# Kernel tuning notes

Measured on AMD Instinct MI355X. Metric: run time of the kernel, lower is better.

Reference implementation:

```python
import jax, jax.numpy as jnp
import numpy as np

N_NODES = 10000
IN_FEAT = 512
OUT_FEAT = 512
N_EDGES = 160000


def setup_inputs() -> dict:
    key = jax.random.key(0)
    kx, kw, ks, kd = jax.random.split(key, 4)
    x = jax.random.normal(kx, (N_NODES, IN_FEAT), dtype=jnp.float32)
    # Xavier-uniform init for w: shape [out_features, 2*in_features]
    fan_in, fan_out = 2 * IN_FEAT, OUT_FEAT
    limit = float(np.sqrt(6.0 / (fan_in + fan_out)))
    w = jax.random.uniform(kw, (OUT_FEAT, 2 * IN_FEAT), dtype=jnp.float32,
                           minval=-limit, maxval=limit)
    src = jax.random.randint(ks, (N_EDGES,), 0, N_NODES, dtype=jnp.int32)
    dst = jax.random.randint(kd, (N_EDGES,), 0, N_NODES, dtype=jnp.int32)
    edge_index = jnp.stack([src, dst], axis=0)  # [2, E]
    return {"x": x, "w": w, "edge_index": edge_index}


def reference(x, w, edge_index):
    # GraphSAGE-mean layer: h = relu(W @ concat(x, mean_{j in N(i)} x_j))
    src, dst = edge_index[0], edge_index[1]
    msgs = x[src]  # [E, F] gather of neighbor features
    summed = jax.ops.segment_sum(msgs, dst, num_segments=x.shape[0])  # [N, F]
    deg = jax.ops.segment_sum(jnp.ones_like(dst, dtype=x.dtype), dst,
                              num_segments=x.shape[0])  # [N]
    neighbor_mean = summed / jnp.maximum(deg, 1.0)[:, None]
    message = jnp.concatenate([x, neighbor_mean], axis=-1)  # [N, 2F]
    weighted = jnp.einsum('of,nf->no', w, message)  # [N, out]
    return jax.nn.relu(weighted)
```

## Files before the change

kernel.cpp:

```cpp
#include <hip/hip_runtime.h>
#include <hip/hip_bf16.h>

#define N_NODES 10000
#define IN_FEAT 512
#define OUT_FEAT 512
#define N_EDGES 160000
#define KDIM 1024
#define CAP 96

typedef __bf16 bf16x8 __attribute__((ext_vector_type(8)));
typedef float f32x4 __attribute__((ext_vector_type(4)));

#define AS1 __attribute__((address_space(1)))
#define AS3 __attribute__((address_space(3)))

__device__ __forceinline__ void async_copy16(void* lds, const void* g) {
    __builtin_amdgcn_global_load_lds((const AS1 unsigned int*)g,
                                     (AS3 unsigned int*)lds, 16, 0, 0);
}

__device__ __forceinline__ unsigned short f2bf(float f) {
    unsigned int u = __builtin_bit_cast(unsigned int, f);
    u += 0x7fffu + ((u >> 16) & 1u);
    return (unsigned short)(u >> 16);
}


__global__ __launch_bounds__(256) void k_zero(int* __restrict__ cnt) {
    int i = blockIdx.x * 256 + threadIdx.x;
    if (i < N_NODES / 4) ((int4*)cnt)[i] = (int4){0, 0, 0, 0};
}


#define PREP_EDGE_BLOCKS ((N_EDGES + 255) / 256)
#define PREP_W_BLOCKS (OUT_FEAT * KDIM / 8 / 256)
#define PREP_X_BLOCKS (N_NODES * IN_FEAT / 8 / 256)
#define PREP_BLOCKS (PREP_EDGE_BLOCKS + PREP_W_BLOCKS + PREP_X_BLOCKS)

__device__ __forceinline__ void cvt8(const float* __restrict__ src,
                                     unsigned short* __restrict__ dst, int i) {
    const float4* sp = (const float4*)(src + (size_t)i * 8);
    float4 a = sp[0], b = sp[1];
    uint4 o;
    o.x = (unsigned)f2bf(a.x) | ((unsigned)f2bf(a.y) << 16);
    o.y = (unsigned)f2bf(a.z) | ((unsigned)f2bf(a.w) << 16);
    o.z = (unsigned)f2bf(b.x) | ((unsigned)f2bf(b.y) << 16);
    o.w = (unsigned)f2bf(b.z) | ((unsigned)f2bf(b.w) << 16);
    *(uint4*)(dst + (size_t)i * 8) = o;
}

__global__ __launch_bounds__(256) void k_prep(
    const float* __restrict__ x, const float* __restrict__ w,
    const int* __restrict__ ei, int* __restrict__ cnt,
    int* __restrict__ bucket, unsigned short* __restrict__ xb,
    unsigned short* __restrict__ wb) {
    int b = blockIdx.x;
    if (b < PREP_EDGE_BLOCKS) {
        int e = b * 256 + threadIdx.x;
        if (e < N_EDGES) {
            int s = ei[e];
            int d = ei[N_EDGES + e];
            int slot = atomicAdd(&cnt[d], 1);
            if (slot < CAP) bucket[d * CAP + slot] = s;
        }
    } else if (b < PREP_EDGE_BLOCKS + PREP_W_BLOCKS) {
        int i = (b - PREP_EDGE_BLOCKS) * 256 + threadIdx.x;
        cvt8(w, wb, i);
    } else {
        int i = (b - PREP_EDGE_BLOCKS - PREP_W_BLOCKS) * 256 + threadIdx.x;
        cvt8(x, xb, i);
    }
}


__device__ __forceinline__ void accum8(float* acc, uint4 v) {
    unsigned d[4] = {v.x, v.y, v.z, v.w};
#pragma unroll
    for (int j = 0; j < 4; ++j) {
        acc[2 * j]     += __builtin_bit_cast(float, d[j] << 16);
        acc[2 * j + 1] += __builtin_bit_cast(float, d[j] & 0xffff0000u);
    }
}

__global__ __launch_bounds__(256) void k_aggregate(
    const unsigned short* __restrict__ xb, const int* __restrict__ cnt,
    const int* __restrict__ bucket, unsigned short* __restrict__ mb) {
    int wid = (blockIdx.x * 256 + threadIdx.x) >> 6;
    int lane = threadIdx.x & 63;
    if (wid >= N_NODES) return;
    int deg = cnt[wid];
    int n = deg < CAP ? deg : CAP;
    const int4* brow = (const int4*)(bucket + wid * CAP);
    const unsigned short* xrow = xb + lane * 8;
    float acc[8] = {0.f, 0.f, 0.f, 0.f, 0.f, 0.f, 0.f, 0.f};
    int e = 0;
    for (; e + 8 <= n; e += 8) {
        int4 i0 = brow[e >> 2];
        int4 i1 = brow[(e >> 2) + 1];
        uint4 v0 = *(const uint4*)(xrow + (size_t)i0.x * IN_FEAT);
        uint4 v1 = *(const uint4*)(xrow + (size_t)i0.y * IN_FEAT);
        uint4 v2 = *(const uint4*)(xrow + (size_t)i0.z * IN_FEAT);
        uint4 v3 = *(const uint4*)(xrow + (size_t)i0.w * IN_FEAT);
        uint4 v4 = *(const uint4*)(xrow + (size_t)i1.x * IN_FEAT);
        uint4 v5 = *(const uint4*)(xrow + (size_t)i1.y * IN_FEAT);
        uint4 v6 = *(const uint4*)(xrow + (size_t)i1.z * IN_FEAT);
        uint4 v7 = *(const uint4*)(xrow + (size_t)i1.w * IN_FEAT);
        accum8(acc, v0); accum8(acc, v1); accum8(acc, v2); accum8(acc, v3);
        accum8(acc, v4); accum8(acc, v5); accum8(acc, v6); accum8(acc, v7);
    }
    if (e + 4 <= n) {
        int4 i0 = brow[e >> 2];
        uint4 v0 = *(const uint4*)(xrow + (size_t)i0.x * IN_FEAT);
        uint4 v1 = *(const uint4*)(xrow + (size_t)i0.y * IN_FEAT);
        uint4 v2 = *(const uint4*)(xrow + (size_t)i0.z * IN_FEAT);
        uint4 v3 = *(const uint4*)(xrow + (size_t)i0.w * IN_FEAT);
        accum8(acc, v0); accum8(acc, v1); accum8(acc, v2); accum8(acc, v3);
        e += 4;
    }
    for (; e < n; ++e) {
        int s = bucket[wid * CAP + e];
        uint4 v = *(const uint4*)(xrow + (size_t)s * IN_FEAT);
        accum8(acc, v);
    }
    float inv = 1.0f / fmaxf((float)deg, 1.0f);
    uint4 o;
    o.x = (unsigned)f2bf(acc[0] * inv) | ((unsigned)f2bf(acc[1] * inv) << 16);
    o.y = (unsigned)f2bf(acc[2] * inv) | ((unsigned)f2bf(acc[3] * inv) << 16);
    o.z = (unsigned)f2bf(acc[4] * inv) | ((unsigned)f2bf(acc[5] * inv) << 16);
    o.w = (unsigned)f2bf(acc[6] * inv) | ((unsigned)f2bf(acc[7] * inv) << 16);
    *(uint4*)(mb + (size_t)wid * IN_FEAT + lane * 8) = o;
}


#define BM 64
#define BN 128
#define BK 64

__global__ __launch_bounds__(256) void k_gemm(const unsigned short* __restrict__ xb,
                                              const unsigned short* __restrict__ mb,
                                              const unsigned short* __restrict__ wb,
                                              float* __restrict__ out) {
    __shared__ unsigned short As[BM * BK];
    __shared__ unsigned short Bs[BN * BK];
    const int tid = threadIdx.x;
    const int lane = tid & 63;
    const int w = tid >> 6;
    const int m0 = blockIdx.x * BM;
    const int n0 = blockIdx.y * BN;

    const int wr = w >> 1, wc = w & 1;

    const int st_sub = lane >> 3;
    const int st_col = ((lane & 7) ^ st_sub) * 8;

    f32x4 acc[2][4];
#pragma unroll
    for (int m = 0; m < 2; ++m)
#pragma unroll
        for (int n = 0; n < 4; ++n) acc[m][n] = (f32x4){0.f, 0.f, 0.f, 0.f};

    for (int k0 = 0; k0 < KDIM; k0 += BK) {
        const unsigned short* abase = (k0 < IN_FEAT) ? xb : mb;
        const int kc = (k0 < IN_FEAT) ? k0 : (k0 - IN_FEAT);
#pragma unroll
        for (int i = 0; i < 2; ++i) {
            int row = w * 16 + i * 8 + st_sub;
            int rg = m0 + row;
            if (rg > N_NODES - 1) rg = N_NODES - 1;
            async_copy16(&As[(w * 16 + i * 8) * BK],
                         abase + (size_t)rg * IN_FEAT + kc + st_col);
        }
#pragma unroll
        for (int i = 0; i < 4; ++i) {
            int row = w * 32 + i * 8 + st_sub;
            async_copy16(&Bs[(w * 32 + i * 8) * BK],
                         wb + (size_t)(n0 + row) * KDIM + k0 + st_col);
        }
        __syncthreads();

#pragma unroll
        for (int kk = 0; kk < 2; ++kk) {
            bf16x8 a[2], b[4];
            const int lslot = kk * 4 + (lane >> 4);
            const int pslot = lslot ^ (lane & 7);
#pragma unroll
            for (int m = 0; m < 2; ++m) {
                int r = wr * 32 + m * 16 + (lane & 15);
                a[m] = *(const bf16x8*)((const char*)As + r * 128 + pslot * 16);
            }
#pragma unroll
            for (int n = 0; n < 4; ++n) {
                int r = wc * 64 + n * 16 + (lane & 15);
                b[n] = *(const bf16x8*)((const char*)Bs + r * 128 + pslot * 16);
            }
#pragma unroll
            for (int m = 0; m < 2; ++m)
#pragma unroll
                for (int n = 0; n < 4; ++n)
                    acc[m][n] = __builtin_amdgcn_mfma_f32_16x16x32_bf16(
                        a[m], b[n], acc[m][n], 0, 0, 0);
        }
        __syncthreads();
    }

    const int col_in = lane & 15;
    const int rquad = (lane >> 4) * 4;
#pragma unroll
    for (int m = 0; m < 2; ++m) {
#pragma unroll
        for (int n = 0; n < 4; ++n) {
#pragma unroll
            for (int r = 0; r < 4; ++r) {
                int mg = m0 + wr * 32 + m * 16 + rquad + r;
                int og = n0 + wc * 64 + n * 16 + col_in;
                if (mg < N_NODES) {
                    float v = acc[m][n][r];
                    out[(size_t)mg * OUT_FEAT + og] = v > 0.f ? v : 0.f;
                }
            }
        }
    }
}


extern "C" void kernel_launch(void* const* d_in, const int* in_sizes, int n_in,
                              void* d_out, int out_size, void* d_ws, size_t ws_size,
                              hipStream_t stream) {
    const float* x = (const float*)d_in[0];
    const float* w = (const float*)d_in[1];
    const int* ei = (const int*)d_in[2];
    float* out = (float*)d_out;

    char* ws = (char*)d_ws;
    const size_t XB_OFF = 0;
    const size_t MB_OFF = XB_OFF + (size_t)N_NODES * IN_FEAT * 2;
    const size_t WB_OFF = MB_OFF + (size_t)N_NODES * IN_FEAT * 2;
    const size_t CNT_OFF = WB_OFF + (size_t)OUT_FEAT * KDIM * 2;
    const size_t BKT_OFF = CNT_OFF + (size_t)N_NODES * 4;

    unsigned short* xb = (unsigned short*)(ws + XB_OFF);
    unsigned short* mb = (unsigned short*)(ws + MB_OFF);
    unsigned short* wb = (unsigned short*)(ws + WB_OFF);
    int* cnt = (int*)(ws + CNT_OFF);
    int* bucket = (int*)(ws + BKT_OFF);

    k_zero<<<(N_NODES / 4 + 255) / 256, 256, 0, stream>>>(cnt);
    k_prep<<<PREP_BLOCKS, 256, 0, stream>>>(x, w, ei, cnt, bucket, xb, wb);
    k_aggregate<<<(N_NODES * 64 + 255) / 256, 256, 0, stream>>>(xb, cnt, bucket, mb);
    dim3 ggrid((N_NODES + BM - 1) / BM, OUT_FEAT / BN);
    k_gemm<<<ggrid, 256, 0, stream>>>(xb, mb, wb, out);
}
```

Measured before the change: 65.55 us.

## Double-buffer GEMM LDS tiles and swizzle block order for L2 reuse

The GEMM kernel now holds two LDS buffers for A and B. The next K-tile's async global-to-LDS copy is issued right after the barrier, so it overlaps with the MFMA work on the current tile, and one barrier per K step is dropped. The 2D grid becomes a 1D grid of 640 blocks, remapped so that groups of 8 M-tiles cycle through all 4 N-tiles together, which is meant to improve L2 reuse of the A rows and the weights. The cost is twice the LDS per block, which may lower occupancy, plus a few idle blocks that exit early.

Measured after the change: 65.88 us. About the same (+0.5%).

```diff
diff --git a/kernel.cpp b/kernel.cpp
--- a/kernel.cpp
+++ b/kernel.cpp
@@ -135,19 +135,25 @@
 #define BM 64
 #define BN 128
 #define BK 64
+#define NSTEP (KDIM / BK)
+#define MT_CNT ((N_NODES + BM - 1) / BM)
 
 __global__ __launch_bounds__(256) void k_gemm(const unsigned short* __restrict__ xb,
                                               const unsigned short* __restrict__ mb,
                                               const unsigned short* __restrict__ wb,
                                               float* __restrict__ out) {
-    __shared__ unsigned short As[BM * BK];
-    __shared__ unsigned short Bs[BN * BK];
+    __shared__ unsigned short As[2][BM * BK];
+    __shared__ unsigned short Bs[2][BN * BK];
+    const int idx = blockIdx.x;
+    const int mt = (idx & 7) + 8 * (idx >> 5);
+    const int nt = (idx >> 3) & 3;
+    if (mt >= MT_CNT) return;
+    const int m0 = mt * BM;
+    const int n0 = nt * BN;
+
     const int tid = threadIdx.x;
     const int lane = tid & 63;
     const int w = tid >> 6;
-    const int m0 = blockIdx.x * BM;
-    const int n0 = blockIdx.y * BN;
-
     const int wr = w >> 1, wc = w & 1;
 
     const int st_sub = lane >> 3;
@@ -159,7 +165,7 @@
 #pragma unroll
         for (int n = 0; n < 4; ++n) acc[m][n] = (f32x4){0.f, 0.f, 0.f, 0.f};
 
-    for (int k0 = 0; k0 < KDIM; k0 += BK) {
+    auto stage = [&](int buf, int k0) {
         const unsigned short* abase = (k0 < IN_FEAT) ? xb : mb;
         const int kc = (k0 < IN_FEAT) ? k0 : (k0 - IN_FEAT);
 #pragma unroll
@@ -167,16 +173,22 @@
             int row = w * 16 + i * 8 + st_sub;
             int rg = m0 + row;
             if (rg > N_NODES - 1) rg = N_NODES - 1;
-            async_copy16(&As[(w * 16 + i * 8) * BK],
+            async_copy16(&As[buf][(w * 16 + i * 8) * BK],
                          abase + (size_t)rg * IN_FEAT + kc + st_col);
         }
 #pragma unroll
         for (int i = 0; i < 4; ++i) {
             int row = w * 32 + i * 8 + st_sub;
-            async_copy16(&Bs[(w * 32 + i * 8) * BK],
+            async_copy16(&Bs[buf][(w * 32 + i * 8) * BK],
                          wb + (size_t)(n0 + row) * KDIM + k0 + st_col);
         }
+    };
+
+    stage(0, 0);
+    int cur = 0;
+    for (int t = 0; t < NSTEP; ++t) {
         __syncthreads();
+        if (t + 1 < NSTEP) stage(cur ^ 1, (t + 1) * BK);
 
 #pragma unroll
         for (int kk = 0; kk < 2; ++kk) {
@@ -186,12 +198,12 @@
 #pragma unroll
             for (int m = 0; m < 2; ++m) {
                 int r = wr * 32 + m * 16 + (lane & 15);
-                a[m] = *(const bf16x8*)((const char*)As + r * 128 + pslot * 16);
+                a[m] = *(const bf16x8*)((const char*)As[cur] + r * 128 + pslot * 16);
             }
 #pragma unroll
             for (int n = 0; n < 4; ++n) {
                 int r = wc * 64 + n * 16 + (lane & 15);
-                b[n] = *(const bf16x8*)((const char*)Bs + r * 128 + pslot * 16);
+                b[n] = *(const bf16x8*)((const char*)Bs[cur] + r * 128 + pslot * 16);
             }
 #pragma unroll
             for (int m = 0; m < 2; ++m)
@@ -200,7 +212,7 @@
                     acc[m][n] = __builtin_amdgcn_mfma_f32_16x16x32_bf16(
                         a[m], b[n], acc[m][n], 0, 0, 0);
         }
-        __syncthreads();
+        cur ^= 1;
     }
 
     const int col_in = lane & 15;
@@ -247,6 +259,5 @@
     k_zero<<<(N_NODES / 4 + 255) / 256, 256, 0, stream>>>(cnt);
     k_prep<<<PREP_BLOCKS, 256, 0, stream>>>(x, w, ei, cnt, bucket, xb, wb);
     k_aggregate<<<(N_NODES * 64 + 255) / 256, 256, 0, stream>>>(xb, cnt, bucket, mb);
-    dim3 ggrid((N_NODES + BM - 1) / BM, OUT_FEAT / BN);
-    k_gemm<<<ggrid, 256, 0, stream>>>(xb, mb, wb, out);
-}
+    k_gemm<<<640, 256, 0, stream>>>(xb, mb, wb, out);
+}
```
